# Kernel tuning notes

Hardware: AMD Instinct MI355X
Metric: run time of the kernel (lower is better)

Reference implementation:

```python
import jax, jax.numpy as jnp
import numpy as np

B, IN_DIM, D, C = 8192, 2048, 1024, 1000


def setup_inputs() -> dict:
    key = jax.random.key(0)
    k1, k2, k3 = jax.random.split(key, 3)
    x = jax.random.normal(k1, (B, IN_DIM), dtype=jnp.float32)
    W_enc = jax.random.normal(k2, (IN_DIM, D), dtype=jnp.float32) * 0.02
    b_enc = jnp.zeros((D,), dtype=jnp.float32)
    prototypes = jax.random.normal(k3, (C, D), dtype=jnp.float32)
    return {"x": x, "W_enc": W_enc, "b_enc": b_enc, "prototypes": prototypes}


def reference(x, W_enc, b_enc, prototypes):
    # Encoder features Z: [B, D] (stand-in for model.forward_encoder)
    Z = x @ W_enc + b_enc
    # MSELoss(Z[i], proto[j]) = mean over D of squared diff
    # = (||z||^2 + ||p||^2 - 2 z.p) / D  -- avoids [B, C, D] intermediate
    z2 = jnp.sum(Z * Z, axis=-1, keepdims=True)          # [B, 1]
    p2 = jnp.sum(prototypes * prototypes, axis=-1)[None]  # [1, C]
    cross = jnp.einsum("bd,cd->bc", Z, prototypes)        # [B, C]
    mse = (z2 + p2 - 2.0 * cross) / jnp.asarray(Z.shape[-1], Z.dtype)
    return -mse
```

## Files before the change

kernel.cpp:

```cpp
#include <hip/hip_runtime.h>

#define B_ROWS 8192
#define IN_DIM 2048
#define D_DIM  1024
#define C_CLS  1000

typedef __attribute__((ext_vector_type(8))) short   bf16x8;
typedef __attribute__((ext_vector_type(4))) float   f32x4;

__device__ __forceinline__ unsigned short f2b(float f) {
    unsigned int u = __builtin_bit_cast(unsigned int, f);
    u = u + 0x7fffu + ((u >> 16) & 1u);
    return (unsigned short)(u >> 16);
}
__device__ __forceinline__ void g2lds16(const void* g, void* l) {
    __builtin_amdgcn_global_load_lds(
        (const __attribute__((address_space(1))) unsigned int*)g,
        (__attribute__((address_space(3))) unsigned int*)l,
        16, 0, 0);
}

__global__ __launch_bounds__(256) void k_pre(const float* __restrict__ W,
                                             const float* __restrict__ P,
                                             const float* __restrict__ x,
                                             unsigned short* __restrict__ Wt,
                                             unsigned short* __restrict__ Pb,
                                             unsigned short* __restrict__ xb,
                                             float* __restrict__ p2) {
    const int tid = threadIdx.x;
    if (blockIdx.x >= 3072) {
        const size_t i = (((size_t)blockIdx.x - 3072) * 256 + tid) * 8;
        float4 v0 = *(const float4*)(x + i);
        float4 v1 = *(const float4*)(x + i + 4);
        bf16x8 h;
        h[0] = (short)f2b(v0.x); h[1] = (short)f2b(v0.y);
        h[2] = (short)f2b(v0.z); h[3] = (short)f2b(v0.w);
        h[4] = (short)f2b(v1.x); h[5] = (short)f2b(v1.y);
        h[6] = (short)f2b(v1.z); h[7] = (short)f2b(v1.w);
        *(bf16x8*)(xb + i) = h;
    } else if (blockIdx.x < 2048) {
        __shared__ float t[32][33];
        const int tx = tid & 31, ty = tid >> 5;
        const int kb = (blockIdx.x & 63) * 32;
        const int nb = (blockIdx.x >> 6) * 32;
#pragma unroll
        for (int j = 0; j < 4; ++j)
            t[ty + 8 * j][tx] = W[(size_t)(kb + ty + 8 * j) * D_DIM + nb + tx];
        __syncthreads();
#pragma unroll
        for (int j = 0; j < 4; ++j)
            Wt[(size_t)(nb + ty + 8 * j) * IN_DIM + kb + tx] = f2b(t[tx][ty + 8 * j]);
    } else {
        const int c = blockIdx.x - 2048;
        float s = 0.f;
        if (c < C_CLS) {
            float4 v = *((const float4*)(P + (size_t)c * D_DIM) + tid);
            s = v.x * v.x + v.y * v.y + v.z * v.z + v.w * v.w;
            ushort4 h; h.x = f2b(v.x); h.y = f2b(v.y); h.z = f2b(v.z); h.w = f2b(v.w);
            *((ushort4*)(Pb + (size_t)c * D_DIM) + tid) = h;
        } else {
            ushort4 h; h.x = 0; h.y = 0; h.z = 0; h.w = 0;
            *((ushort4*)(Pb + (size_t)c * D_DIM) + tid) = h;
        }
#pragma unroll
        for (int o = 32; o > 0; o >>= 1) s += __shfl_down(s, o);
        __shared__ float red[4];
        if ((tid & 63) == 0) red[tid >> 6] = s;
        __syncthreads();
        if (tid == 0) p2[c] = red[0] + red[1] + red[2] + red[3];
    }
}

template <int MODE>
__global__ __launch_bounds__(256, 2) void k_gemm(
    const unsigned short* __restrict__ Ab,
    const unsigned short* __restrict__ Bt,
    const float* __restrict__ bias,
    const float* __restrict__ z2p_in,
    const float* __restrict__ p2,
    unsigned short* __restrict__ Zout,
    float* __restrict__ z2p_out,
    float* __restrict__ Out) {
    constexpr int K  = (MODE == 0) ? IN_DIM : D_DIM;
    constexpr int NT = K / 64;
    constexpr unsigned SSZ = 128 * 64 * 2;
    extern __shared__ char lds[];
    char* pa0 = lds;             char* pa1 = lds + SSZ;
    char* pa2 = lds + 2 * SSZ;
    char* pb0 = (MODE == 0) ? lds + 3 * SSZ : lds + 2 * SSZ;
    char* pb1 = pb0 + SSZ;
    float* z2loc = (float*)(lds + 4 * SSZ);

    const int tid  = threadIdx.x;
    const int wave = tid >> 6, lane = tid & 63;
    const int lo = lane & 15, hi = lane >> 4;
    const int wm = wave >> 1, wn = wave & 1;

    const int swz = (blockIdx.x & 7) * 64 + (blockIdx.x >> 3);
    const int bm = swz >> 3, bn = swz & 7;
    const int rowbase = bm * 128, colbase = bn * 128;

    const int srow   = lane >> 3;
    const int gchunk = (lane & 7) ^ (srow & 7);

    auto STAGE_A = [&](char* dst, int kt) {
#pragma unroll
        for (int i = 0; i < 4; ++i) {
            const int s = i * 4 + wave;
            g2lds16(Ab + (size_t)(rowbase + s * 8 + srow) * K + kt * 64 + gchunk * 8,
                    dst + s * 1024);
        }
    };
    auto STAGE_B = [&](char* dst, int kt) {
#pragma unroll
        for (int i = 0; i < 4; ++i) {
            const int s = i * 4 + wave;
            g2lds16(Bt + (size_t)(colbase + s * 8 + srow) * K + kt * 64 + gchunk * 8,
                    dst + s * 1024);
        }
    };

    f32x4 acc[4][4];
#pragma unroll
    for (int m = 0; m < 4; ++m)
#pragma unroll
        for (int n = 0; n < 4; ++n) acc[m][n] = (f32x4){0.f, 0.f, 0.f, 0.f};

    if constexpr (MODE == 0) {
        STAGE_A(pa0, 0);
        STAGE_B(pb0, 0);
        STAGE_A(pa1, 1);
        asm volatile("s_waitcnt vmcnt(4) lgkmcnt(0)" ::: "memory");
    } else {
        if (tid < 128) {
            float s = 0.f;
#pragma unroll
            for (int j = 0; j < 16; ++j) s += z2p_in[j * B_ROWS + rowbase + tid];
            z2loc[tid] = s;
        }
        STAGE_A(pa0, 0);
        STAGE_B(pb0, 0);
        asm volatile("s_waitcnt vmcnt(0) lgkmcnt(0)" ::: "memory");
    }
    __builtin_amdgcn_s_barrier();

    auto COMPUTE = [&]() {
#pragma unroll
        for (int ks = 0; ks < 2; ++ks) {
            bf16x8 af[4], bfr[4];
#pragma unroll
            for (int m = 0; m < 4; ++m) {
                const int row = wm * 64 + m * 16 + lo;
                unsigned addr = (unsigned)(row * 128 + ks * 64 + hi * 16)
                              ^ (unsigned)((lo & 7) << 4);
                af[m] = *(const bf16x8*)(pa0 + addr);
            }
#pragma unroll
            for (int n = 0; n < 4; ++n) {
                const int row = wn * 64 + n * 16 + lo;
                unsigned addr = (unsigned)(row * 128 + ks * 64 + hi * 16)
                              ^ (unsigned)((lo & 7) << 4);
                bfr[n] = *(const bf16x8*)(pb0 + addr);
            }
            __builtin_amdgcn_s_setprio(1);
#pragma unroll
            for (int m = 0; m < 4; ++m)
#pragma unroll
                for (int n = 0; n < 4; ++n)
                    acc[m][n] = __builtin_amdgcn_mfma_f32_16x16x32_bf16(
                        af[m], bfr[n], acc[m][n], 0, 0, 0);
            __builtin_amdgcn_s_setprio(0);
        }
    };

    if constexpr (MODE == 0) {
        for (int t = 0; t < NT; ++t) {
            if (t + 1 < NT) STAGE_B(pb1, t + 1);
            if (t + 2 < NT) STAGE_A(pa2, t + 2);
            COMPUTE();
            if (t < NT - 1) {
                if (t + 2 < NT)
                    asm volatile("s_waitcnt vmcnt(4)" ::: "memory");
                else
                    asm volatile("s_waitcnt vmcnt(0)" ::: "memory");
                __builtin_amdgcn_s_barrier();
                char* ta = pa0; pa0 = pa1; pa1 = pa2; pa2 = ta;
                char* tb = pb0; pb0 = pb1; pb1 = tb;
            }
        }
    } else {
        for (int t = 0; t < NT; ++t) {
            const bool nx = (t + 1 < NT);
            if (nx) {
                STAGE_A(pa1, t + 1);
                STAGE_B(pb1, t + 1);
            }
            COMPUTE();
            if (nx) {
                asm volatile("s_waitcnt vmcnt(0)" ::: "memory");
                __builtin_amdgcn_s_barrier();
                char* ta = pa0; pa0 = pa1; pa1 = ta;
                char* tb = pb0; pb0 = pb1; pb1 = tb;
            }
        }
    }

    if constexpr (MODE == 0) {
        float bv[4];
#pragma unroll
        for (int n = 0; n < 4; ++n) bv[n] = bias[colbase + wn * 64 + n * 16 + lo];
#pragma unroll
        for (int m = 0; m < 4; ++m)
#pragma unroll
            for (int r = 0; r < 4; ++r) {
                const int rg = rowbase + wm * 64 + m * 16 + hi * 4 + r;
                float s = 0.f;
#pragma unroll
                for (int n = 0; n < 4; ++n) {
                    const float zf = acc[m][n][r] + bv[n];
                    Zout[(size_t)rg * D_DIM + colbase + wn * 64 + n * 16 + lo] = f2b(zf);
                    s += zf * zf;
                }
                s += __shfl_xor(s, 1); s += __shfl_xor(s, 2);
                s += __shfl_xor(s, 4); s += __shfl_xor(s, 8);
                if (lo == 0) z2p_out[(size_t)(bn * 2 + wn) * B_ROWS + rg] = s;
            }
    } else {
        float p2v[4];
#pragma unroll
        for (int n = 0; n < 4; ++n) p2v[n] = p2[colbase + wn * 64 + n * 16 + lo];
#pragma unroll
        for (int m = 0; m < 4; ++m)
#pragma unroll
            for (int r = 0; r < 4; ++r) {
                const int rl = wm * 64 + m * 16 + hi * 4 + r;
                const int rg = rowbase + rl;
                const float zv = z2loc[rl];
#pragma unroll
                for (int n = 0; n < 4; ++n) {
                    const int cg = colbase + wn * 64 + n * 16 + lo;
                    if (cg < C_CLS)
                        Out[(size_t)rg * C_CLS + cg] =
                            (2.f * acc[m][n][r] - zv - p2v[n]) * (1.f / 1024.f);
                }
            }
    }
}

extern "C" void kernel_launch(void* const* d_in, const int* in_sizes, int n_in,
                              void* d_out, int out_size, void* d_ws, size_t ws_size,
                              hipStream_t stream) {
    const float* x = (const float*)d_in[0];
    const float* W = (const float*)d_in[1];
    const float* b = (const float*)d_in[2];
    const float* P = (const float*)d_in[3];
    float* out = (float*)d_out;

    char* ws = (char*)d_ws;
    unsigned short* Wt  = (unsigned short*)(ws);
    unsigned short* Pb  = (unsigned short*)(ws + (4  << 20));
    unsigned short* Zb  = (unsigned short*)(ws + (6  << 20));
    float*          p2  = (float*)(ws + (22 << 20) + (64 << 10));
    float*          z2p = (float*)(ws + (22 << 20) + (128 << 10));
    unsigned short* xb  = (unsigned short*)(ws + (23 << 20));

    const unsigned lds0 = 5 * (128 * 64 * 2);
    const unsigned lds1 = 4 * (128 * 64 * 2) + 512;

    k_pre<<<dim3(11264), dim3(256), 0, stream>>>(W, P, x, Wt, Pb, xb, p2);
    k_gemm<0><<<dim3(512), dim3(256), lds0, stream>>>(
        xb, Wt, b, nullptr, nullptr, Zb, z2p, nullptr);
    k_gemm<1><<<dim3(512), dim3(256), lds1, stream>>>(
        Zb, Pb, nullptr, z2p, p2, nullptr, nullptr, out);
}
```

Baseline: 81.57 us.

## Store GEMM operands in pre-tiled 128x64 blocked layout for contiguous tile loads

The preprocessing kernel and the first GEMM's Z output now write x, W^T, prototypes and Z in a blocked layout. Each 128-row by 64-column tile becomes a contiguous 16 KB slab. The GEMM staging loads then read fully contiguous memory per K-step instead of 128 strided rows, which improves DRAM/TLB locality for the direct global-to-LDS loads. The cost is scattered, less coalesced writes in the prep kernel and the Z epilogue, and every stage must agree on the tile layout.

```diff
diff --git a/kernel.cpp b/kernel.cpp
--- a/kernel.cpp
+++ b/kernel.cpp
@@ -19,6 +19,7 @@
         (__attribute__((address_space(3))) unsigned int*)l,
         16, 0, 0);
 }
+
 
 __global__ __launch_bounds__(256) void k_pre(const float* __restrict__ W,
                                              const float* __restrict__ P,
@@ -29,15 +30,18 @@
                                              float* __restrict__ p2) {
     const int tid = threadIdx.x;
     if (blockIdx.x >= 3072) {
-        const size_t i = (((size_t)blockIdx.x - 3072) * 256 + tid) * 8;
-        float4 v0 = *(const float4*)(x + i);
-        float4 v1 = *(const float4*)(x + i + 4);
+        const size_t e = (((size_t)blockIdx.x - 3072) * 256 + tid) * 8;
+        const int row = (int)(e >> 11), k = (int)(e & 2047);
+        float4 v0 = *(const float4*)(x + e);
+        float4 v1 = *(const float4*)(x + e + 4);
         bf16x8 h;
         h[0] = (short)f2b(v0.x); h[1] = (short)f2b(v0.y);
         h[2] = (short)f2b(v0.z); h[3] = (short)f2b(v0.w);
         h[4] = (short)f2b(v1.x); h[5] = (short)f2b(v1.y);
         h[6] = (short)f2b(v1.z); h[7] = (short)f2b(v1.w);
-        *(bf16x8*)(xb + i) = h;
+        const size_t dst = ((size_t)((row >> 7) * 32 + (k >> 6))) * 8192
+                         + (row & 127) * 64 + (k & 63);
+        *(bf16x8*)(xb + dst) = h;
     } else if (blockIdx.x < 2048) {
         __shared__ float t[32][33];
         const int tx = tid & 31, ty = tid >> 5;
@@ -48,19 +52,26 @@
             t[ty + 8 * j][tx] = W[(size_t)(kb + ty + 8 * j) * D_DIM + nb + tx];
         __syncthreads();
 #pragma unroll
-        for (int j = 0; j < 4; ++j)
-            Wt[(size_t)(nb + ty + 8 * j) * IN_DIM + kb + tx] = f2b(t[tx][ty + 8 * j]);
+        for (int j = 0; j < 4; ++j) {
+            const int n = nb + ty + 8 * j, k = kb + tx;
+            const size_t dst = ((size_t)((n >> 7) * 32 + (k >> 6))) * 8192
+                             + (n & 127) * 64 + (k & 63);
+            Wt[dst] = f2b(t[tx][ty + 8 * j]);
+        }
     } else {
         const int c = blockIdx.x - 2048;
+        const int d = tid * 4;
+        const size_t dst = ((size_t)((c >> 7) * 16 + (d >> 6))) * 8192
+                         + (c & 127) * 64 + (d & 63);
         float s = 0.f;
         if (c < C_CLS) {
             float4 v = *((const float4*)(P + (size_t)c * D_DIM) + tid);
             s = v.x * v.x + v.y * v.y + v.z * v.z + v.w * v.w;
             ushort4 h; h.x = f2b(v.x); h.y = f2b(v.y); h.z = f2b(v.z); h.w = f2b(v.w);
-            *((ushort4*)(Pb + (size_t)c * D_DIM) + tid) = h;
+            *(ushort4*)(Pb + dst) = h;
         } else {
             ushort4 h; h.x = 0; h.y = 0; h.z = 0; h.w = 0;
-            *((ushort4*)(Pb + (size_t)c * D_DIM) + tid) = h;
+            *(ushort4*)(Pb + dst) = h;
         }
 #pragma unroll
         for (int o = 32; o > 0; o >>= 1) s += __shfl_down(s, o);
@@ -102,21 +113,25 @@
 
     const int srow   = lane >> 3;
     const int gchunk = (lane & 7) ^ (srow & 7);
+    const int soff   = srow * 64 + gchunk * 8;
+
+    const unsigned short* Aslab = Ab + (size_t)bm * NT * 8192;
+    const unsigned short* Bslab = Bt + (size_t)bn * NT * 8192;
 
     auto STAGE_A = [&](char* dst, int kt) {
+        const unsigned short* base = Aslab + (size_t)kt * 8192;
 #pragma unroll
         for (int i = 0; i < 4; ++i) {
             const int s = i * 4 + wave;
-            g2lds16(Ab + (size_t)(rowbase + s * 8 + srow) * K + kt * 64 + gchunk * 8,
-                    dst + s * 1024);
+            g2lds16(base + s * 512 + soff, dst + s * 1024);
         }
     };
     auto STAGE_B = [&](char* dst, int kt) {
+        const unsigned short* base = Bslab + (size_t)kt * 8192;
 #pragma unroll
         for (int i = 0; i < 4; ++i) {
             const int s = i * 4 + wave;
-            g2lds16(Bt + (size_t)(colbase + s * 8 + srow) * K + kt * 64 + gchunk * 8,
-                    dst + s * 1024);
+            g2lds16(base + s * 512 + soff, dst + s * 1024);
         }
     };
 
@@ -213,12 +228,15 @@
         for (int m = 0; m < 4; ++m)
 #pragma unroll
             for (int r = 0; r < 4; ++r) {
-                const int rg = rowbase + wm * 64 + m * 16 + hi * 4 + r;
+                const int rl = wm * 64 + m * 16 + hi * 4 + r;
+                const int rg = rowbase + rl;
                 float s = 0.f;
 #pragma unroll
                 for (int n = 0; n < 4; ++n) {
                     const float zf = acc[m][n][r] + bv[n];
-                    Zout[(size_t)rg * D_DIM + colbase + wn * 64 + n * 16 + lo] = f2b(zf);
+                    const size_t dst = ((size_t)(bm * 16 + bn * 2 + wn)) * 8192
+                                     + rl * 64 + n * 16 + lo;
+                    Zout[dst] = f2b(zf);
                     s += zf * zf;
                 }
                 s += __shfl_xor(s, 1); s += __shfl_xor(s, 2);
```

Result: no change. 82.10 us (+0.6%).
